# Kernel optimization log

Hardware: AMD Instinct MI355X
Metric: run time of the kernel (lower is better)

The kernel has to match this reference:

```python
import jax, jax.numpy as jnp
import numpy as np

E, K, D = 50000, 8, 256
NH = 4
HD = D // NH
SCALE = HD ** -0.5
EPS = 1e-8


def setup_inputs() -> dict:
    key = jax.random.key(0)
    ks = jax.random.split(key, 16)
    p = lambda k, shp: (jax.random.normal(k, shp, dtype=jnp.float32) * 0.02)
    return {
        "x_i": jax.random.normal(ks[0], (E, D), dtype=jnp.float32),
        "x_j": jax.random.normal(ks[1], (E, D), dtype=jnp.float32),
        "h_seq_i": jax.random.normal(ks[2], (E, K, D), dtype=jnp.float32),
        "h_seq_j": jax.random.normal(ks[3], (E, K, D), dtype=jnp.float32),
        "edge_emb": jax.random.normal(ks[4], (E, D), dtype=jnp.float32),
        "Wq": p(ks[5], (D, D)), "bq": jnp.zeros((D,), jnp.float32),
        "Wk": p(ks[6], (D, D)), "bk": jnp.zeros((D,), jnp.float32),
        "We1": p(ks[7], (D, D // 2)), "be1": jnp.zeros((D // 2,), jnp.float32),
        "We2": p(ks[8], (D // 2, 1)), "be2": jnp.zeros((1,), jnp.float32),
        "Wo1": p(ks[9], (3, 16)), "bo1": jnp.zeros((16,), jnp.float32),
        "Wo2": p(ks[10], (16, 1)), "bo2": jnp.zeros((1,), jnp.float32),
    }


def reference(x_i, x_j, h_seq_i, h_seq_j, edge_emb,
              Wq, bq, Wk, bk, We1, be1, We2, be2, Wo1, bo1, Wo2, bo2):
    # (A) attribute alignment: cosine similarity mapped to (0,1)
    num = jnp.sum(x_i * x_j, axis=-1)
    den = jnp.maximum(jnp.linalg.norm(x_i, axis=-1), EPS) * \
          jnp.maximum(jnp.linalg.norm(x_j, axis=-1), EPS)
    attr_score = (num / den + 1.0) / 2.0  # [E]

    # (B) activity alignment: tiny cross-attention, mean of softmax diagonal
    Q = (jnp.einsum('ekd,df->ekf', h_seq_i, Wq) + bq).reshape(E, K, NH, HD)
    Kv = (jnp.einsum('ekd,df->ekf', h_seq_j, Wk) + bk).reshape(E, K, NH, HD)
    scores = jnp.einsum('eqhd,ekhd->ehqk', Q, Kv) * SCALE  # [E,NH,K,K]
    attn = jax.nn.softmax(scores, axis=-1)
    diag = jnp.diagonal(attn, axis1=-2, axis2=-1)  # [E,NH,K]
    activity_score = diag.mean(axis=(-1, -2))  # [E]

    # (C) edge plausibility MLP (exact GELU as in torch default)
    h = jax.nn.gelu(edge_emb @ We1 + be1, approximate=False)
    edge_score = jax.nn.sigmoid((h @ We2 + be2)[..., 0])  # [E]

    signals = jnp.stack([attr_score, activity_score, edge_score], axis=-1)  # [E,3]
    out = jax.nn.gelu(signals @ Wo1 + bo1, approximate=False) @ Wo2 + bo2
    return jax.nn.sigmoid(out[..., 0])  # [E]
```

## Files before the change

### kernel.cpp

```cpp
#include <hip/hip_runtime.h>

#define E_TOT   50000
#define DD      256
#define EPG     8
#define NWG     (E_TOT / EPG)
#define SCALE_V 0.125f

#define NHCHUNK 12800000
#define NECHUNK 1600000

typedef __attribute__((ext_vector_type(4))) float f32x4;
typedef __attribute__((ext_vector_type(8))) short short8;

__device__ __forceinline__ unsigned short f2bf(float f) {
    unsigned u = __float_as_uint(f);
    u += 0x7fffu + ((u >> 16) & 1u);
    return (unsigned short)(u >> 16);
}
__device__ __forceinline__ float gelu_exact(float x) {
    return 0.5f * x * (1.0f + erff(x * 0.70710678118654752440f));
}
__device__ __forceinline__ float sigmoidf(float x) {
    return 1.0f / (1.0f + __expf(-x));
}

__device__ __forceinline__ void dma16(const void* g, void* lds) {
    const int lane = threadIdx.x & 63;
    auto gp = (const __attribute__((address_space(1))) char*)g + lane * 16;
    auto lp = (__attribute__((address_space(3))) char*)lds;
    __builtin_amdgcn_global_load_lds(gp, lp, 16, 0, 0);
}

__global__ void prep_weights(const float* __restrict__ Wq,
                             const float* __restrict__ Wk,
                             const float* __restrict__ We1,
                             unsigned short* __restrict__ wqT,
                             unsigned short* __restrict__ wkT,
                             unsigned short* __restrict__ w1T) {
    int i = blockIdx.x * 256 + threadIdx.x;
    if (i < 65536) {
        int k = i >> 8, n = i & 255;
        wqT[n * 256 + k] = f2bf(Wq[i]);
    } else if (i < 131072) {
        int j = i - 65536;
        int k = j >> 8, n = j & 255;
        wkT[n * 256 + k] = f2bf(Wk[j]);
    } else {
        int j = i - 131072;
        int k = j >> 7, n = j & 127;
        w1T[n * 256 + k] = f2bf(We1[j]);
    }
}

__global__ void conv_frag(const float* __restrict__ hi,
                          const float* __restrict__ hj,
                          const float* __restrict__ emb,
                          unsigned short* __restrict__ fi,
                          unsigned short* __restrict__ fj,
                          unsigned short* __restrict__ ebf) {
    const int nthr = gridDim.x * blockDim.x;
    const int tid  = blockIdx.x * blockDim.x + threadIdx.x;

    for (int c = tid; c < NHCHUNK; c += nthr) {
        const int g  = c >> 10;
        const int r  = c & 1023;
        const int ks = r >> 7, m = (r >> 6) & 1, l = r & 63;
        const size_t row = (size_t)g * 32 + m * 16 + (l & 15);
        const int    col = ks * 32 + (l >> 4) * 8;
        const float* pi = hi + row * DD + col;
        const float* pj = hj + row * DD + col;
        f32x4 a0 = *(const f32x4*)pi;
        f32x4 a1 = *(const f32x4*)(pi + 4);
        f32x4 b0 = *(const f32x4*)pj;
        f32x4 b1 = *(const f32x4*)(pj + 4);
        *(ushort4*)(fi + (size_t)c * 8)     =
            make_ushort4(f2bf(a0[0]), f2bf(a0[1]), f2bf(a0[2]), f2bf(a0[3]));
        *(ushort4*)(fi + (size_t)c * 8 + 4) =
            make_ushort4(f2bf(a1[0]), f2bf(a1[1]), f2bf(a1[2]), f2bf(a1[3]));
        *(ushort4*)(fj + (size_t)c * 8)     =
            make_ushort4(f2bf(b0[0]), f2bf(b0[1]), f2bf(b0[2]), f2bf(b0[3]));
        *(ushort4*)(fj + (size_t)c * 8 + 4) =
            make_ushort4(f2bf(b1[0]), f2bf(b1[1]), f2bf(b1[2]), f2bf(b1[3]));
    }
    for (int c = tid; c < NECHUNK; c += nthr) {
        const float* p = emb + (size_t)c * 8;
        f32x4 a0 = *(const f32x4*)p;
        f32x4 a1 = *(const f32x4*)(p + 4);
        *(ushort4*)(ebf + (size_t)c * 8)     =
            make_ushort4(f2bf(a0[0]), f2bf(a0[1]), f2bf(a0[2]), f2bf(a0[3]));
        *(ushort4*)(ebf + (size_t)c * 8 + 4) =
            make_ushort4(f2bf(a1[0]), f2bf(a1[1]), f2bf(a1[2]), f2bf(a1[3]));
    }
}

__device__ __forceinline__ void writeback4(unsigned short (*T)[260],
                                           const f32x4 acc[4][4],
                                           const float* __restrict__ bias,
                                           int lr, int lq, int w) {
    #pragma unroll
    for (int n = 0; n < 4; ++n) {
        const int col = (w * 4 + n) * 16 + lr;
        const float bs = bias[col];
        #pragma unroll
        for (int m = 0; m < 4; ++m) {
            #pragma unroll
            for (int v = 0; v < 4; ++v) {
                const int row = m * 16 + lq * 4 + v;
                T[row][col] = f2bf(acc[m][n][v] + bs);
            }
        }
    }
}

__global__ __launch_bounds__(256, 2)
void fused_tile(const float* __restrict__ x_i,
                const float* __restrict__ x_j,
                const unsigned short* __restrict__ fi,
                const unsigned short* __restrict__ fj,
                const unsigned short* __restrict__ ebf,
                const unsigned short* __restrict__ wqT,
                const unsigned short* __restrict__ wkT,
                const unsigned short* __restrict__ w1T,
                const float* __restrict__ bq,
                const float* __restrict__ bk,
                const float* __restrict__ be1,
                const float* __restrict__ We2,
                const float* __restrict__ be2,
                const float* __restrict__ Wo1,
                const float* __restrict__ bo1,
                const float* __restrict__ Wo2,
                const float* __restrict__ bo2,
                float* __restrict__ out) {
    __shared__ __align__(16) unsigned char lds[66560 + 128];
    unsigned short (*tQ)[260] = (unsigned short (*)[260])lds;
    unsigned short (*tK)[260] = (unsigned short (*)[260])(lds + 33280);
    unsigned char* fiS = lds;
    unsigned char* fjS = lds + 33280;
    float* sEdgeP = (float*)(lds + 66560);

    const int t  = threadIdx.x;
    const int w  = t >> 6;
    const int l  = t & 63;
    const int lr = l & 15, lq = l >> 4;
    const int b  = blockIdx.x;

    #pragma unroll
    for (int i = 0; i < 8; ++i)
        dma16((const char*)fi + (size_t)b * 32768 + w * 8192 + i * 1024,
              fiS + w * 8192 + i * 1024);
    #pragma unroll
    for (int i = 0; i < 8; ++i)
        dma16((const char*)fj + (size_t)b * 32768 + w * 8192 + i * 1024,
              fjS + w * 8192 + i * 1024);

    float attr[2];
    #pragma unroll
    for (int ee = 0; ee < 2; ++ee) {
        const int e = b * EPG + 2 * w + ee;
        f32x4 xa = *(const f32x4*)(x_i + (size_t)e * DD + l * 4);
        f32x4 xb = *(const f32x4*)(x_j + (size_t)e * DD + l * 4);
        float cd = xa[0]*xb[0] + xa[1]*xb[1] + xa[2]*xb[2] + xa[3]*xb[3];
        float ci = xa[0]*xa[0] + xa[1]*xa[1] + xa[2]*xa[2] + xa[3]*xa[3];
        float cj = xb[0]*xb[0] + xb[1]*xb[1] + xb[2]*xb[2] + xb[3]*xb[3];
        #pragma unroll
        for (int off = 1; off < 64; off <<= 1) {
            cd += __shfl_xor(cd, off);
            ci += __shfl_xor(ci, off);
            cj += __shfl_xor(cj, off);
        }
        attr[ee] = (cd / (fmaxf(sqrtf(ci), 1e-8f) * fmaxf(sqrtf(cj), 1e-8f))
                    + 1.0f) * 0.5f;
    }

    {
        f32x4 accE[2] = {};
        const unsigned short* er = ebf + ((size_t)b * EPG + (lr & 7)) * 256;
        #pragma unroll
        for (int ks = 0; ks < 8; ++ks) {
            short8 ae = *(const short8*)(er + ks * 32 + lq * 8);
            #pragma unroll
            for (int n = 0; n < 2; ++n) {
                const int col = w * 32 + n * 16 + lr;
                short8 bv = *(const short8*)(w1T + col * 256 + ks * 32 + lq * 8);
                accE[n] = __builtin_amdgcn_mfma_f32_16x16x32_bf16(ae, bv, accE[n], 0, 0, 0);
            }
        }
        float p[4] = {0.f, 0.f, 0.f, 0.f};
        #pragma unroll
        for (int n = 0; n < 2; ++n) {
            const int col = w * 32 + n * 16 + lr;
            const float b1 = be1[col], w2 = We2[col];
            #pragma unroll
            for (int v = 0; v < 4; ++v)
                p[v] += gelu_exact(accE[n][v] + b1) * w2;
        }
        #pragma unroll
        for (int off = 1; off < 16; off <<= 1) {
            #pragma unroll
            for (int v = 0; v < 4; ++v) p[v] += __shfl_xor(p[v], off);
        }
        if (l == 0) {
            sEdgeP[w * 8 + 0] = p[0]; sEdgeP[w * 8 + 1] = p[1];
            sEdgeP[w * 8 + 2] = p[2]; sEdgeP[w * 8 + 3] = p[3];
        }
        if (l == 16) {
            sEdgeP[w * 8 + 4] = p[0]; sEdgeP[w * 8 + 5] = p[1];
            sEdgeP[w * 8 + 6] = p[2]; sEdgeP[w * 8 + 7] = p[3];
        }
    }
    __syncthreads();

    f32x4 accQ[4][4] = {};
    #pragma unroll
    for (int ks = 0; ks < 8; ++ks) {
        short8 bv[4];
        #pragma unroll
        for (int n = 0; n < 4; ++n)
            bv[n] = *(const short8*)(wqT + ((w * 4 + n) * 16 + lr) * 256 + ks * 32 + lq * 8);
        #pragma unroll
        for (int m = 0; m < 4; ++m) {
            short8 av = *(const short8*)(fiS + (m >> 1) * 16384 + ks * 2048 +
                                         (m & 1) * 1024 + l * 16);
            #pragma unroll
            for (int n = 0; n < 4; ++n)
                accQ[m][n] = __builtin_amdgcn_mfma_f32_16x16x32_bf16(av, bv[n], accQ[m][n], 0, 0, 0);
        }
    }
    __syncthreads();
    writeback4(tQ, accQ, bq, lr, lq, w);

    f32x4 accK[4][4] = {};
    #pragma unroll
    for (int ks = 0; ks < 8; ++ks) {
        short8 bv[4];
        #pragma unroll
        for (int n = 0; n < 4; ++n)
            bv[n] = *(const short8*)(wkT + ((w * 4 + n) * 16 + lr) * 256 + ks * 32 + lq * 8);
        #pragma unroll
        for (int m = 0; m < 4; ++m) {
            short8 av = *(const short8*)(fjS + (m >> 1) * 16384 + ks * 2048 +
                                         (m & 1) * 1024 + l * 16);
            #pragma unroll
            for (int n = 0; n < 4; ++n)
                accK[m][n] = __builtin_amdgcn_mfma_f32_16x16x32_bf16(av, bv[n], accK[m][n], 0, 0, 0);
        }
    }
    __syncthreads();
    writeback4(tK, accK, bk, lr, lq, w);
    __syncthreads();

    float contrib[2] = {0.f, 0.f};
    #pragma unroll
    for (int ee = 0; ee < 2; ++ee) {
        const int rowb = (2 * w + ee) * 8 + (lr & 7);
        #pragma unroll
        for (int h = 0; h < 4; ++h) {
            f32x4 s = {};
            #pragma unroll
            for (int ks = 0; ks < 2; ++ks) {
                short8 a = *(const short8*)&tK[rowb][h * 64 + ks * 32 + lq * 8];
                short8 bb = *(const short8*)&tQ[rowb][h * 64 + ks * 32 + lq * 8];
                s = __builtin_amdgcn_mfma_f32_16x16x32_bf16(a, bb, s, 0, 0, 0);
            }
            float sc[4];
            #pragma unroll
            for (int v = 0; v < 4; ++v) sc[v] = s[v] * SCALE_V;
            float m4 = fmaxf(fmaxf(sc[0], sc[1]), fmaxf(sc[2], sc[3]));
            float mx = fmaxf(m4, __shfl_xor(m4, 16));
            float pe[4], ps = 0.f;
            #pragma unroll
            for (int v = 0; v < 4; ++v) { pe[v] = __expf(sc[v] - mx); ps += pe[v]; }
            float tot = ps + __shfl_xor(ps, 16);
            float pd = 0.f;
            #pragma unroll
            for (int v = 0; v < 4; ++v)
                pd = (((lq * 4 + v) & 7) == (lr & 7)) ? pe[v] : pd;
            if (lr < 8 && lq < 2) contrib[ee] += pd / tot;
        }
    }
    #pragma unroll
    for (int off = 1; off < 64; off <<= 1) {
        contrib[0] += __shfl_xor(contrib[0], off);
        contrib[1] += __shfl_xor(contrib[1], off);
    }

    #pragma unroll
    for (int ee = 0; ee < 2; ++ee) {
        const int eloc = 2 * w + ee;
        const float act = contrib[ee] * (1.0f / 32.0f);
        const float es  = sigmoidf(sEdgeP[0 * 8 + eloc] + sEdgeP[1 * 8 + eloc] +
                                   sEdgeP[2 * 8 + eloc] + sEdgeP[3 * 8 + eloc] + be2[0]);
        float r = 0.f;
        if (l < 16) {
            float z = attr[ee] * Wo1[l] + act * Wo1[16 + l] + es * Wo1[32 + l] + bo1[l];
            r = gelu_exact(z) * Wo2[l];
        }
        r += __shfl_xor(r, 1);
        r += __shfl_xor(r, 2);
        r += __shfl_xor(r, 4);
        r += __shfl_xor(r, 8);
        if (l == 0) out[b * EPG + eloc] = sigmoidf(r + bo2[0]);
    }
}

extern "C" void kernel_launch(void* const* d_in, const int* in_sizes, int n_in,
                              void* d_out, int out_size, void* d_ws, size_t ws_size,
                              hipStream_t stream) {
    const float* x_i  = (const float*)d_in[0];
    const float* x_j  = (const float*)d_in[1];
    const float* h_i  = (const float*)d_in[2];
    const float* h_j  = (const float*)d_in[3];
    const float* emb  = (const float*)d_in[4];
    const float* Wq   = (const float*)d_in[5];
    const float* bq   = (const float*)d_in[6];
    const float* Wk   = (const float*)d_in[7];
    const float* bk   = (const float*)d_in[8];
    const float* We1  = (const float*)d_in[9];
    const float* be1  = (const float*)d_in[10];
    const float* We2  = (const float*)d_in[11];
    const float* be2  = (const float*)d_in[12];
    const float* Wo1  = (const float*)d_in[13];
    const float* bo1  = (const float*)d_in[14];
    const float* Wo2  = (const float*)d_in[15];
    const float* bo2  = (const float*)d_in[16];
    float* out = (float*)d_out;

    unsigned short* wqT = (unsigned short*)d_ws;
    unsigned short* wkT = wqT + 65536;
    unsigned short* w1T = wkT + 65536;
    unsigned short* ebf = w1T + 32768;
    unsigned short* fi  = ebf + 12800000;
    unsigned short* fj  = fi + 102400000;

    prep_weights<<<640, 256, 0, stream>>>(Wq, Wk, We1, wqT, wkT, w1T);
    conv_frag<<<2048, 256, 0, stream>>>(h_i, h_j, emb, fi, fj, ebf);
    fused_tile<<<NWG, 256, 0, stream>>>(x_i, x_j, fi, fj, ebf,
                                        wqT, wkT, w1T,
                                        bq, bk, be1, We2, be2,
                                        Wo1, bo1, Wo2, bo2, out);
}
```

Before: 674.8 us.

## Halve edges per workgroup and interleave Q/K projections for higher occupancy

Each workgroup now handles 4 edges instead of 8, which halves the LDS footprint and raises the launch-bounds occupancy target from 2 to 4 blocks per CU. The Q and K projections are computed together in one k-loop, sharing the weight-fragment loop structure, so one barrier-separated phase is removed. The cosine reduction is also merged into the final shuffle reduction. In exchange, each weight fragment is reused across fewer rows, so global/L2 weight traffic per edge doubles, and the edge-MLP MFMA now wastes half its rows (lr&3 duplicates).

After: 849.2 us. 1.26x slower.

```diff
diff --git a/kernel.cpp b/kernel.cpp
--- a/kernel.cpp
+++ b/kernel.cpp
@@ -2,7 +2,7 @@
 
 #define E_TOT   50000
 #define DD      256
-#define EPG     8
+#define EPG     4
 #define NWG     (E_TOT / EPG)
 #define SCALE_V 0.125f
 
@@ -93,8 +93,8 @@
     }
 }
 
-__device__ __forceinline__ void writeback4(unsigned short (*T)[260],
-                                           const f32x4 acc[4][4],
+__device__ __forceinline__ void writeback2(unsigned short (*T)[260],
+                                           const f32x4 acc[2][4],
                                            const float* __restrict__ bias,
                                            int lr, int lq, int w) {
     #pragma unroll
@@ -102,7 +102,7 @@
         const int col = (w * 4 + n) * 16 + lr;
         const float bs = bias[col];
         #pragma unroll
-        for (int m = 0; m < 4; ++m) {
+        for (int m = 0; m < 2; ++m) {
             #pragma unroll
             for (int v = 0; v < 4; ++v) {
                 const int row = m * 16 + lq * 4 + v;
@@ -112,8 +112,8 @@
     }
 }
 
-__global__ __launch_bounds__(256, 2)
-void fused_tile(const float* __restrict__ x_i,
+__global__ __launch_bounds__(256, 4)
+void fused_lite(const float* __restrict__ x_i,
                 const float* __restrict__ x_j,
                 const unsigned short* __restrict__ fi,
                 const unsigned short* __restrict__ fj,
@@ -131,50 +131,41 @@
                 const float* __restrict__ Wo2,
                 const float* __restrict__ bo2,
                 float* __restrict__ out) {
-    __shared__ __align__(16) unsigned char lds[66560 + 128];
+    __shared__ __align__(16) unsigned char lds[33344];
     unsigned short (*tQ)[260] = (unsigned short (*)[260])lds;
-    unsigned short (*tK)[260] = (unsigned short (*)[260])(lds + 33280);
+    unsigned short (*tK)[260] = (unsigned short (*)[260])(lds + 16640);
     unsigned char* fiS = lds;
-    unsigned char* fjS = lds + 33280;
-    float* sEdgeP = (float*)(lds + 66560);
+    unsigned char* fjS = lds + 16640;
+    float* sEdgeP = (float*)(lds + 33280);
 
     const int t  = threadIdx.x;
     const int w  = t >> 6;
     const int l  = t & 63;
     const int lr = l & 15, lq = l >> 4;
     const int b  = blockIdx.x;
-
-    #pragma unroll
-    for (int i = 0; i < 8; ++i)
-        dma16((const char*)fi + (size_t)b * 32768 + w * 8192 + i * 1024,
-              fiS + w * 8192 + i * 1024);
-    #pragma unroll
-    for (int i = 0; i < 8; ++i)
-        dma16((const char*)fj + (size_t)b * 32768 + w * 8192 + i * 1024,
-              fjS + w * 8192 + i * 1024);
-
-    float attr[2];
-    #pragma unroll
-    for (int ee = 0; ee < 2; ++ee) {
-        const int e = b * EPG + 2 * w + ee;
+    const int e  = b * EPG + w;
+
+    #pragma unroll
+    for (int i = 0; i < 4; ++i)
+        dma16((const char*)fi + (size_t)b * 16384 + w * 4096 + i * 1024,
+              fiS + w * 4096 + i * 1024);
+    #pragma unroll
+    for (int i = 0; i < 4; ++i)
+        dma16((const char*)fj + (size_t)b * 16384 + w * 4096 + i * 1024,
+              fjS + w * 4096 + i * 1024);
+
+    float cd, ci, cj;
+    {
         f32x4 xa = *(const f32x4*)(x_i + (size_t)e * DD + l * 4);
         f32x4 xb = *(const f32x4*)(x_j + (size_t)e * DD + l * 4);
-        float cd = xa[0]*xb[0] + xa[1]*xb[1] + xa[2]*xb[2] + xa[3]*xb[3];
-        float ci = xa[0]*xa[0] + xa[1]*xa[1] + xa[2]*xa[2] + xa[3]*xa[3];
-        float cj = xb[0]*xb[0] + xb[1]*xb[1] + xb[2]*xb[2] + xb[3]*xb[3];
-        #pragma unroll
-        for (int off = 1; off < 64; off <<= 1) {
-            cd += __shfl_xor(cd, off);
-            ci += __shfl_xor(ci, off);
-            cj += __shfl_xor(cj, off);
-        }
-        attr[ee] = (cd / (fmaxf(sqrtf(ci), 1e-8f) * fmaxf(sqrtf(cj), 1e-8f))
-                    + 1.0f) * 0.5f;
-    }
-
+        cd = xa[0]*xb[0] + xa[1]*xb[1] + xa[2]*xb[2] + xa[3]*xb[3];
+        ci = xa[0]*xa[0] + xa[1]*xa[1] + xa[2]*xa[2] + xa[3]*xa[3];
+        cj = xb[0]*xb[0] + xb[1]*xb[1] + xb[2]*xb[2] + xb[3]*xb[3];
+    }
+
+    f32x4 accE[2] = {};
     {
-        f32x4 accE[2] = {};
-        const unsigned short* er = ebf + ((size_t)b * EPG + (lr & 7)) * 256;
+        const unsigned short* er = ebf + ((size_t)b * EPG + (lr & 3)) * 256;
         #pragma unroll
         for (int ks = 0; ks < 8; ++ks) {
             short8 ae = *(const short8*)(er + ks * 32 + lq * 8);
@@ -185,6 +176,8 @@
                 accE[n] = __builtin_amdgcn_mfma_f32_16x16x32_bf16(ae, bv, accE[n], 0, 0, 0);
             }
         }
+    }
+    {
         float p[4] = {0.f, 0.f, 0.f, 0.f};
         #pragma unroll
         for (int n = 0; n < 2; ++n) {
@@ -200,107 +193,84 @@
             for (int v = 0; v < 4; ++v) p[v] += __shfl_xor(p[v], off);
         }
         if (l == 0) {
-            sEdgeP[w * 8 + 0] = p[0]; sEdgeP[w * 8 + 1] = p[1];
-            sEdgeP[w * 8 + 2] = p[2]; sEdgeP[w * 8 + 3] = p[3];
-        }
-        if (l == 16) {
-            sEdgeP[w * 8 + 4] = p[0]; sEdgeP[w * 8 + 5] = p[1];
-            sEdgeP[w * 8 + 6] = p[2]; sEdgeP[w * 8 + 7] = p[3];
+            sEdgeP[w * 4 + 0] = p[0]; sEdgeP[w * 4 + 1] = p[1];
+            sEdgeP[w * 4 + 2] = p[2]; sEdgeP[w * 4 + 3] = p[3];
         }
     }
     __syncthreads();
 
-    f32x4 accQ[4][4] = {};
+    f32x4 accQ[2][4] = {};
+    f32x4 accK[2][4] = {};
     #pragma unroll
     for (int ks = 0; ks < 8; ++ks) {
-        short8 bv[4];
-        #pragma unroll
-        for (int n = 0; n < 4; ++n)
-            bv[n] = *(const short8*)(wqT + ((w * 4 + n) * 16 + lr) * 256 + ks * 32 + lq * 8);
-        #pragma unroll
-        for (int m = 0; m < 4; ++m) {
-            short8 av = *(const short8*)(fiS + (m >> 1) * 16384 + ks * 2048 +
-                                         (m & 1) * 1024 + l * 16);
-            #pragma unroll
-            for (int n = 0; n < 4; ++n)
-                accQ[m][n] = __builtin_amdgcn_mfma_f32_16x16x32_bf16(av, bv[n], accQ[m][n], 0, 0, 0);
+        #pragma unroll
+        for (int n = 0; n < 4; ++n) {
+            const int cb = ((w * 4 + n) * 16 + lr) * 256 + ks * 32 + lq * 8;
+            short8 bq8 = *(const short8*)(wqT + cb);
+            short8 bk8 = *(const short8*)(wkT + cb);
+            #pragma unroll
+            for (int m = 0; m < 2; ++m) {
+                short8 ai = *(const short8*)(fiS + ks * 2048 + m * 1024 + l * 16);
+                short8 aj = *(const short8*)(fjS + ks * 2048 + m * 1024 + l * 16);
+                accQ[m][n] = __builtin_amdgcn_mfma_f32_16x16x32_bf16(ai, bq8, accQ[m][n], 0, 0, 0);
+                accK[m][n] = __builtin_amdgcn_mfma_f32_16x16x32_bf16(aj, bk8, accK[m][n], 0, 0, 0);
+            }
         }
     }
     __syncthreads();
-    writeback4(tQ, accQ, bq, lr, lq, w);
-
-    f32x4 accK[4][4] = {};
-    #pragma unroll
-    for (int ks = 0; ks < 8; ++ks) {
-        short8 bv[4];
-        #pragma unroll
-        for (int n = 0; n < 4; ++n)
-            bv[n] = *(const short8*)(wkT + ((w * 4 + n) * 16 + lr) * 256 + ks * 32 + lq * 8);
-        #pragma unroll
-        for (int m = 0; m < 4; ++m) {
-            short8 av = *(const short8*)(fjS + (m >> 1) * 16384 + ks * 2048 +
-                                         (m & 1) * 1024 + l * 16);
-            #pragma unroll
-            for (int n = 0; n < 4; ++n)
-                accK[m][n] = __builtin_amdgcn_mfma_f32_16x16x32_bf16(av, bv[n], accK[m][n], 0, 0, 0);
-        }
-    }
+    writeback2(tQ, accQ, bq, lr, lq, w);
+    writeback2(tK, accK, bk, lr, lq, w);
     __syncthreads();
-    writeback4(tK, accK, bk, lr, lq, w);
-    __syncthreads();
-
-    float contrib[2] = {0.f, 0.f};
-    #pragma unroll
-    for (int ee = 0; ee < 2; ++ee) {
-        const int rowb = (2 * w + ee) * 8 + (lr & 7);
-        #pragma unroll
-        for (int h = 0; h < 4; ++h) {
-            f32x4 s = {};
-            #pragma unroll
-            for (int ks = 0; ks < 2; ++ks) {
-                short8 a = *(const short8*)&tK[rowb][h * 64 + ks * 32 + lq * 8];
-                short8 bb = *(const short8*)&tQ[rowb][h * 64 + ks * 32 + lq * 8];
-                s = __builtin_amdgcn_mfma_f32_16x16x32_bf16(a, bb, s, 0, 0, 0);
-            }
-            float sc[4];
-            #pragma unroll
-            for (int v = 0; v < 4; ++v) sc[v] = s[v] * SCALE_V;
-            float m4 = fmaxf(fmaxf(sc[0], sc[1]), fmaxf(sc[2], sc[3]));
-            float mx = fmaxf(m4, __shfl_xor(m4, 16));
-            float pe[4], ps = 0.f;
-            #pragma unroll
-            for (int v = 0; v < 4; ++v) { pe[v] = __expf(sc[v] - mx); ps += pe[v]; }
-            float tot = ps + __shfl_xor(ps, 16);
-            float pd = 0.f;
-            #pragma unroll
-            for (int v = 0; v < 4; ++v)
-                pd = (((lq * 4 + v) & 7) == (lr & 7)) ? pe[v] : pd;
-            if (lr < 8 && lq < 2) contrib[ee] += pd / tot;
-        }
-    }
+
+    float contrib = 0.f;
+    #pragma unroll
+    for (int h = 0; h < 4; ++h) {
+        f32x4 s = {};
+        #pragma unroll
+        for (int ks = 0; ks < 2; ++ks) {
+            short8 a  = *(const short8*)&tK[w * 8 + (lr & 7)][h * 64 + ks * 32 + lq * 8];
+            short8 bb = *(const short8*)&tQ[w * 8 + (lr & 7)][h * 64 + ks * 32 + lq * 8];
+            s = __builtin_amdgcn_mfma_f32_16x16x32_bf16(a, bb, s, 0, 0, 0);
+        }
+        float sc[4];
+        #pragma unroll
+        for (int v = 0; v < 4; ++v) sc[v] = s[v] * SCALE_V;
+        float m4 = fmaxf(fmaxf(sc[0], sc[1]), fmaxf(sc[2], sc[3]));
+        float mx = fmaxf(m4, __shfl_xor(m4, 16));
+        float pe[4], ps = 0.f;
+        #pragma unroll
+        for (int v = 0; v < 4; ++v) { pe[v] = __expf(sc[v] - mx); ps += pe[v]; }
+        float tot = ps + __shfl_xor(ps, 16);
+        float pd = 0.f;
+        #pragma unroll
+        for (int v = 0; v < 4; ++v)
+            pd = (((lq * 4 + v) & 7) == (lr & 7)) ? pe[v] : pd;
+        if (lr < 8 && lq < 2) contrib += pd / tot;
+    }
+
     #pragma unroll
     for (int off = 1; off < 64; off <<= 1) {
-        contrib[0] += __shfl_xor(contrib[0], off);
-        contrib[1] += __shfl_xor(contrib[1], off);
-    }
-
-    #pragma unroll
-    for (int ee = 0; ee < 2; ++ee) {
-        const int eloc = 2 * w + ee;
-        const float act = contrib[ee] * (1.0f / 32.0f);
-        const float es  = sigmoidf(sEdgeP[0 * 8 + eloc] + sEdgeP[1 * 8 + eloc] +
-                                   sEdgeP[2 * 8 + eloc] + sEdgeP[3 * 8 + eloc] + be2[0]);
-        float r = 0.f;
-        if (l < 16) {
-            float z = attr[ee] * Wo1[l] + act * Wo1[16 + l] + es * Wo1[32 + l] + bo1[l];
-            r = gelu_exact(z) * Wo2[l];
-        }
-        r += __shfl_xor(r, 1);
-        r += __shfl_xor(r, 2);
-        r += __shfl_xor(r, 4);
-        r += __shfl_xor(r, 8);
-        if (l == 0) out[b * EPG + eloc] = sigmoidf(r + bo2[0]);
-    }
+        contrib += __shfl_xor(contrib, off);
+        cd += __shfl_xor(cd, off);
+        ci += __shfl_xor(ci, off);
+        cj += __shfl_xor(cj, off);
+    }
+    const float act  = contrib * (1.0f / 32.0f);
+    const float attr = (cd / (fmaxf(sqrtf(ci), 1e-8f) * fmaxf(sqrtf(cj), 1e-8f))
+                        + 1.0f) * 0.5f;
+    const float es = sigmoidf(sEdgeP[0 * 4 + w] + sEdgeP[1 * 4 + w] +
+                              sEdgeP[2 * 4 + w] + sEdgeP[3 * 4 + w] + be2[0]);
+
+    float r = 0.f;
+    if (l < 16) {
+        float z = attr * Wo1[l] + act * Wo1[16 + l] + es * Wo1[32 + l] + bo1[l];
+        r = gelu_exact(z) * Wo2[l];
+    }
+    r += __shfl_xor(r, 1);
+    r += __shfl_xor(r, 2);
+    r += __shfl_xor(r, 4);
+    r += __shfl_xor(r, 8);
+    if (l == 0) out[e] = sigmoidf(r + bo2[0]);
 }
 
 extern "C" void kernel_launch(void* const* d_in, const int* in_sizes, int n_in,
@@ -334,7 +304,7 @@
 
     prep_weights<<<640, 256, 0, stream>>>(Wq, Wk, We1, wqT, wkT, w1T);
     conv_frag<<<2048, 256, 0, stream>>>(h_i, h_j, emb, fi, fj, ebf);
-    fused_tile<<<NWG, 256, 0, stream>>>(x_i, x_j, fi, fj, ebf,
+    fused_lite<<<NWG, 256, 0, stream>>>(x_i, x_j, fi, fj, ebf,
                                         wqT, wkT, w1T,
                                         bq, bk, be1, We2, be2,
                                         Wo1, bo1, Wo2, bo2, out);
```
